# Performance work log

Measured on AMD Instinct MI355X. Metric: run time of the kernel, lower is better.

Reference implementation:

```python
import jax, jax.numpy as jnp
import numpy as np

N_HEAD = 16
SIZE_PER_HEAD = 64
NEG_BIG = 1e12


def _len_mask(lengths, T):
    # Faithful to: mask = 1 - cumsum(one_hot(len, T), 1)
    # -> 1.0 for positions < len, 0.0 for positions >= len (all ones if len == T).
    pos = jnp.arange(T)
    return (pos[None, :] < lengths[:, 0, None]).astype(jnp.float32)  # [B, T]


def setup_inputs() -> dict:
    key = jax.random.key(0)
    ks = jax.random.split(key, 8)
    B, T, D = 2, 2048, 1024
    Q_seq = jax.random.normal(ks[0], (B, T, D), dtype=jnp.float32)
    K_seq = jax.random.normal(ks[1], (B, T, D), dtype=jnp.float32)
    V_seq = jax.random.normal(ks[2], (B, T, D), dtype=jnp.float32)
    Q_len = jax.random.randint(ks[3], (B, 1), 0, T, dtype=jnp.int32)
    V_len = jax.random.randint(ks[4], (B, 1), 0, T, dtype=jnp.int32)
    s = 1.0 / np.sqrt(D)
    WQ = jax.random.normal(ks[5], (D, N_HEAD * SIZE_PER_HEAD), dtype=jnp.float32) * s
    WK = jax.random.normal(ks[6], (D, N_HEAD * SIZE_PER_HEAD), dtype=jnp.float32) * s
    WV = jax.random.normal(ks[7], (D, N_HEAD * SIZE_PER_HEAD), dtype=jnp.float32) * s
    return {"Q_seq": Q_seq, "K_seq": K_seq, "V_seq": V_seq,
            "Q_len": Q_len, "V_len": V_len, "WQ": WQ, "WK": WK, "WV": WV}


def reference(Q_seq, K_seq, V_seq, Q_len, V_len, WQ, WK, WV):
    B, Tq, _ = Q_seq.shape
    Tk = K_seq.shape[1]
    H, dh = N_HEAD, SIZE_PER_HEAD

    q = (Q_seq @ WQ).reshape(B, Tq, H, dh)  # [B,Tq,H,dh]
    k = (K_seq @ WK).reshape(B, Tk, H, dh)
    v = (V_seq @ WV).reshape(B, Tk, H, dh)

    # scaled dot-product scores [B,H,Tq,Tk]
    A = jnp.einsum('bqhd,bkhd->bhqk', q, k) / np.sqrt(dh).astype(np.float32)

    # additive key-length mask over the key axis (original: permute+mask+permute)
    kmask = _len_mask(V_len, Tk)  # [B,Tk]
    A = A - (1.0 - kmask)[:, None, None, :] * NEG_BIG
    A = jax.nn.softmax(A, axis=-1)

    O = jnp.einsum('bhqk,bkhd->bqhd', A, v).reshape(B, Tq, H * dh)

    # multiplicative query-length mask
    qmask = _len_mask(Q_len, Tq)  # [B,Tq]
    return O * qmask[:, :, None]
```

## Files before the change

### kernel.cpp

```cpp
#include <hip/hip_runtime.h>


using short8   = __attribute__((ext_vector_type(8))) short;
using floatx4  = __attribute__((ext_vector_type(4))) float;
using floatx16 = __attribute__((ext_vector_type(16))) float;
using uintx4   = __attribute__((ext_vector_type(4))) unsigned int;
using ushort4v = __attribute__((ext_vector_type(4))) unsigned short;

__device__ __forceinline__ unsigned short f2bf(float f) {
    unsigned int u = __builtin_bit_cast(unsigned int, f);
    u += 0x7fffu + ((u >> 16) & 1u);
    return (unsigned short)(u >> 16);
}

__global__ __launch_bounds__(256) void cvt_kernel(
    const float* __restrict__ Qs, const float* __restrict__ Ks,
    const float* __restrict__ Vs, const int* __restrict__ Qlen,
    const int* __restrict__ Vlen, unsigned short* __restrict__ abf)
{
    int z = blockIdx.y, row = blockIdx.x;
    int b = row >> 11, rib = row & 2047;
    int ql = Qlen[b]; int vl = Vlen[b]; int vle = vl ? vl : 2048;
    int lim = (z == 0) ? ((ql + 127) & ~127) : ((vle + 127) & ~127);
    if (rib >= lim) return;
    const float* src = (z == 0) ? Qs : ((z == 1) ? Ks : Vs);
    int t = threadIdx.x;
    float4 v = *reinterpret_cast<const float4*>(src + (size_t)row * 1024 + t * 4);
    ushort4v o;
    o[0] = f2bf(v.x); o[1] = f2bf(v.y); o[2] = f2bf(v.z); o[3] = f2bf(v.w);
    *reinterpret_cast<ushort4v*>(abf + (size_t)z * 4194304u + (size_t)row * 1024 + t * 4) = o;
}

__global__ __launch_bounds__(256) void wt_kernel(
    const float* __restrict__ W0, const float* __restrict__ W1,
    const float* __restrict__ W2, unsigned short* __restrict__ out)
{
    __shared__ float tile[64][65];
    int z = blockIdx.z;
    const float* W = (z == 0) ? W0 : ((z == 1) ? W1 : W2);
    unsigned short* O = out + (size_t)z * 1048576u;
    int r0 = blockIdx.y * 64, c0 = blockIdx.x * 64;
    int t = threadIdx.x;
#pragma unroll
    for (int i = 0; i < 16; i++) {
        int idx = t + i * 256; int r = idx >> 6, c = idx & 63;
        tile[r][c] = W[(size_t)(r0 + r) * 1024 + c0 + c];
    }
    __syncthreads();
#pragma unroll
    for (int i = 0; i < 16; i++) {
        int idx = t + i * 256; int c = idx >> 6, r = idx & 63;
        O[(size_t)(c0 + c) * 1024 + r0 + r] = f2bf(tile[r][c]);
    }
}

template <bool PRECVT>
__global__ __launch_bounds__(256) void proj_kernel(
    const float* __restrict__ Qs, const float* __restrict__ Ks,
    const float* __restrict__ Vs, const unsigned short* __restrict__ abf,
    const unsigned short* __restrict__ wt,
    const int* __restrict__ Qlen, const int* __restrict__ Vlen,
    unsigned short* __restrict__ q, unsigned short* __restrict__ k,
    unsigned short* __restrict__ vh)
{
    __shared__ alignas(16) unsigned short As[128][72];
    __shared__ alignas(16) unsigned short Bs[128][72];

    int z = blockIdx.z;
    int tid = threadIdx.x;
    int m0 = blockIdx.y * 128, n0 = blockIdx.x * 128;
    int b = m0 >> 11, rib = m0 & 2047;
    int ql = Qlen[b]; int vl = Vlen[b]; int vle = vl ? vl : 2048;
    int lim = (z == 0) ? ((ql + 127) & ~127) : ((vle + 127) & ~127);
    if (rib >= lim) return;

    const float* Af = (z == 0) ? Qs : ((z == 1) ? Ks : Vs);
    const unsigned short* Ab = abf + (size_t)z * 4194304u;
    const unsigned short* Bt = wt + (size_t)z * 1048576u;

    int w = tid >> 6, lane = tid & 63, g = lane >> 4, lr = lane & 15;
    int wr = w >> 1, wc = w & 1;

    floatx4 acc[4][4];
#pragma unroll
    for (int m = 0; m < 4; m++)
#pragma unroll
        for (int n = 0; n < 4; n++) {
#pragma unroll
            for (int r = 0; r < 4; r++) acc[m][n][r] = 0.f;
        }

    int srow = tid >> 1, scol = (tid & 1) * 32;

    short8 pa[4], pb[4];
    float4 fa[8];

    if constexpr (PRECVT) {
#pragma unroll
        for (int i = 0; i < 4; i++)
            pa[i] = *reinterpret_cast<const short8*>(Ab + (size_t)(m0 + srow) * 1024 + scol + i * 8);
    } else {
#pragma unroll
        for (int i = 0; i < 8; i++)
            fa[i] = *reinterpret_cast<const float4*>(Af + (size_t)(m0 + srow) * 1024 + scol + i * 4);
    }
#pragma unroll
    for (int i = 0; i < 4; i++)
        pb[i] = *reinterpret_cast<const short8*>(Bt + (size_t)(n0 + srow) * 1024 + scol + i * 8);

    for (int kb = 0; kb < 1024; kb += 64) {
        __syncthreads();
        if constexpr (PRECVT) {
#pragma unroll
            for (int i = 0; i < 4; i++)
                *reinterpret_cast<short8*>(&As[srow][scol + i * 8]) = pa[i];
        } else {
#pragma unroll
            for (int i = 0; i < 4; i++) {
                short8 hcv;
                hcv[0] = (short)f2bf(fa[2*i].x);   hcv[1] = (short)f2bf(fa[2*i].y);
                hcv[2] = (short)f2bf(fa[2*i].z);   hcv[3] = (short)f2bf(fa[2*i].w);
                hcv[4] = (short)f2bf(fa[2*i+1].x); hcv[5] = (short)f2bf(fa[2*i+1].y);
                hcv[6] = (short)f2bf(fa[2*i+1].z); hcv[7] = (short)f2bf(fa[2*i+1].w);
                *reinterpret_cast<short8*>(&As[srow][scol + i * 8]) = hcv;
            }
        }
#pragma unroll
        for (int i = 0; i < 4; i++)
            *reinterpret_cast<short8*>(&Bs[srow][scol + i * 8]) = pb[i];
        __syncthreads();

        if (kb + 64 < 1024) {
            if constexpr (PRECVT) {
#pragma unroll
                for (int i = 0; i < 4; i++)
                    pa[i] = *reinterpret_cast<const short8*>(Ab + (size_t)(m0 + srow) * 1024 + kb + 64 + scol + i * 8);
            } else {
#pragma unroll
                for (int i = 0; i < 8; i++)
                    fa[i] = *reinterpret_cast<const float4*>(Af + (size_t)(m0 + srow) * 1024 + kb + 64 + scol + i * 4);
            }
#pragma unroll
            for (int i = 0; i < 4; i++)
                pb[i] = *reinterpret_cast<const short8*>(Bt + (size_t)(n0 + srow) * 1024 + kb + 64 + scol + i * 8);
        }

#pragma unroll
        for (int kc = 0; kc < 2; kc++) {
            short8 af[4], bf[4];
#pragma unroll
            for (int m = 0; m < 4; m++)
                af[m] = *reinterpret_cast<const short8*>(&As[wr * 64 + m * 16 + lr][kc * 32 + g * 8]);
#pragma unroll
            for (int n = 0; n < 4; n++)
                bf[n] = *reinterpret_cast<const short8*>(&Bs[wc * 64 + n * 16 + lr][kc * 32 + g * 8]);
#pragma unroll
            for (int m = 0; m < 4; m++)
#pragma unroll
                for (int n = 0; n < 4; n++)
                    acc[m][n] = __builtin_amdgcn_mfma_f32_16x16x32_bf16(af[m], bf[n], acc[m][n], 0, 0, 0);
        }
    }

    if (z < 2) {
        unsigned short* outp = (z == 0) ? q : k;
#pragma unroll
        for (int m = 0; m < 4; m++) {
            int row0 = m0 + wr * 64 + m * 16 + g * 4;
            int tb = row0 & 2047;
            int tile = tb >> 6, rin = tb & 63;
#pragma unroll
            for (int n = 0; n < 4; n++) {
                int col = n0 + wc * 64 + n * 16 + lr;
                int hh = col >> 6, dd = col & 63;
                int cc = dd >> 4, h2 = (dd >> 3) & 1, u = dd & 7;
                size_t base = ((size_t)(b * 16 + hh) * 32 + tile) * 4096
                            + (size_t)((cc * 2 + h2) * 512) + (size_t)rin * 8 + u;
#pragma unroll
                for (int r = 0; r < 4; r++)
                    outp[base + (size_t)r * 8] = f2bf(acc[m][n][r]);
            }
        }
    } else {
#pragma unroll
        for (int m = 0; m < 4; m++) {
            int row0 = m0 + wr * 64 + m * 16 + g * 4;
            int tg = row0 & 2047;
            int tile = tg >> 6, kin = tg & 63;
            int cc = kin >> 4, h2 = (kin >> 3) & 1, u = kin & 7;
#pragma unroll
            for (int n = 0; n < 4; n++) {
                int col = n0 + wc * 64 + n * 16 + lr;
                int hh = col >> 6, dd = col & 63;
                ushort4v pk;
#pragma unroll
                for (int r = 0; r < 4; r++) pk[r] = f2bf(acc[m][n][r]);
                size_t addr = ((size_t)(b * 16 + hh) * 32 + tile) * 4096
                            + (size_t)((cc * 2 + h2) * 512) + (size_t)dd * 8 + u;
                *reinterpret_cast<ushort4v*>(vh + addr) = pk;
            }
        }
    }
}

__global__ __launch_bounds__(128) void attn_kernel(
    const unsigned short* __restrict__ q, const unsigned short* __restrict__ k,
    const unsigned short* __restrict__ vh, const int* __restrict__ Qlen,
    const int* __restrict__ Vlen, float* __restrict__ out)
{
    __shared__ float obuf[2][64][33];
    __shared__ float mlm[2][2][33];
    __shared__ float mll[2][2][33];

    int tid = threadIdx.x;
    int w = tid >> 6, lane = tid & 63;
    int j = lane & 31, hi = lane >> 5;

    int blk = blockIdx.x;
    int x = blk & 7, idx = blk >> 3;
    int bh = x + 8 * (idx >> 5), qb = idx & 31;
    int b = bh >> 4, h = bh & 15;
    int qlen = Qlen[b]; int vl = Vlen[b]; int vle = vl ? vl : 2048;

    if (qb * 64 >= qlen) {
        int zr = qb * 64 + (tid >> 1);
        float* p = out + (size_t)(b * 2048 + zr) * 1024 + h * 64 + (tid & 1) * 32;
        float4 z4; z4.x = 0.f; z4.y = 0.f; z4.z = 0.f; z4.w = 0.f;
#pragma unroll
        for (int s = 0; s < 8; s++) *reinterpret_cast<float4*>(p + 4 * s) = z4;
        return;
    }

    int nt = (vle + 63) >> 6;
    int ntw = (nt - w + 1) >> 1;

    size_t hb = (size_t)(b * 16 + h) * 131072u;
    const unsigned short* kh = k + hb;
    const unsigned short* vb = vh + hb;
    int lo = hi * 512 + j * 8;

    short8 qfA[4], qfB[4];
    {
        const unsigned short* qt = q + hb + (size_t)qb * 4096 + lo;
#pragma unroll
        for (int c = 0; c < 4; c++) {
            qfA[c] = *reinterpret_cast<const short8*>(qt + c * 1024);
            qfB[c] = *reinterpret_cast<const short8*>(qt + c * 1024 + 256);
        }
    }

    short8 kf0[4], kf1[4], vf0[4], vf1[4];
    {
        int t0 = (w < nt) ? w : (nt - 1);
        const unsigned short* kt0 = kh + (size_t)t0 * 4096 + lo;
        const unsigned short* vt0 = vb + (size_t)t0 * 4096 + lo;
#pragma unroll
        for (int c = 0; c < 4; c++) {
            kf0[c] = *reinterpret_cast<const short8*>(kt0 + c * 1024);
            kf1[c] = *reinterpret_cast<const short8*>(kt0 + c * 1024 + 256);
            vf0[c] = *reinterpret_cast<const short8*>(vt0 + c * 1024);
            vf1[c] = *reinterpret_cast<const short8*>(vt0 + c * 1024 + 256);
        }
    }
    __builtin_amdgcn_sched_barrier(0);

    floatx16 OA0, OA1, OB0, OB1;
#pragma unroll
    for (int t = 0; t < 16; t++) { OA0[t] = 0.f; OA1[t] = 0.f; OB0[t] = 0.f; OB1[t] = 0.f; }
    float mA = -3.0e38f, lA = 0.f, mB = -3.0e38f, lB = 0.f;

    const float CEXP = 0.18033688011112042f;

    for (int mi = 0; mi < ntw; ++mi) {
        int tix = w + 2 * mi;
        int kt = tix << 6;
        int tnx = tix + 2; if (tnx >= nt) tnx = nt - 1;

        floatx16 s0, s1;
#pragma unroll
        for (int t = 0; t < 16; t++) { s0[t] = 0.f; s1[t] = 0.f; }
#pragma unroll
        for (int c = 0; c < 4; c++) {
            s0 = __builtin_amdgcn_mfma_f32_32x32x16_bf16(kf0[c], qfA[c], s0, 0, 0, 0);
            s1 = __builtin_amdgcn_mfma_f32_32x32x16_bf16(kf1[c], qfA[c], s1, 0, 0, 0);
        }
        if (kt + 64 > vle) {
#pragma unroll
            for (int t = 0; t < 16; t++) {
                int kl = (t & 3) + 8 * (t >> 2) + 4 * hi;
                if (kt + kl >= vle)      s0[t] = -8.0e12f;
                if (kt + 32 + kl >= vle) s1[t] = -8.0e12f;
            }
        }
        {
            float mx = s0[0];
#pragma unroll
            for (int t = 1; t < 16; t++) mx = fmaxf(mx, s0[t]);
#pragma unroll
            for (int t = 0; t < 16; t++) mx = fmaxf(mx, s1[t]);
            float lm = fmaxf(mx, __shfl_xor(mx, 32));
            if (__any(lm > mA + 64.f)) {
                float mn = fmaxf(mA, lm);
                float al = __builtin_amdgcn_exp2f((mA - mn) * CEXP);
                mA = mn; lA *= al;
#pragma unroll
                for (int t = 0; t < 16; t++) { OA0[t] *= al; OA1[t] *= al; }
            }
            float nm = -mA * CEXP;
#pragma unroll
            for (int t = 0; t < 16; t++) {
                s0[t] = __builtin_amdgcn_exp2f(fmaf(s0[t], CEXP, nm));
                s1[t] = __builtin_amdgcn_exp2f(fmaf(s1[t], CEXP, nm));
            }
            float rs = 0.f;
#pragma unroll
            for (int t = 0; t < 16; t++) rs += s0[t] + s1[t];
            lA += rs;
        }
        {
            unsigned int pbw[4][4];
            unsigned int D[4][2];
#pragma unroll
            for (int s = 0; s < 4; s++) {
                asm("v_cvt_pk_bf16_f32 %0, %1, %2" : "=v"(D[s][0]) : "v"(s0[4*s+0]), "v"(s0[4*s+1]));
                asm("v_cvt_pk_bf16_f32 %0, %1, %2" : "=v"(D[s][1]) : "v"(s0[4*s+2]), "v"(s0[4*s+3]));
            }
#pragma unroll
            for (int u = 0; u < 2; u++) {
                asm volatile("v_permlane32_swap_b32 %0, %1" : "+v"(D[0][u]), "+v"(D[1][u]));
                asm volatile("v_permlane32_swap_b32 %0, %1" : "+v"(D[2][u]), "+v"(D[3][u]));
                pbw[0][u] = D[0][u]; pbw[0][u + 2] = D[1][u];
                pbw[1][u] = D[2][u]; pbw[1][u + 2] = D[3][u];
            }
#pragma unroll
            for (int s = 0; s < 4; s++) {
                asm("v_cvt_pk_bf16_f32 %0, %1, %2" : "=v"(D[s][0]) : "v"(s1[4*s+0]), "v"(s1[4*s+1]));
                asm("v_cvt_pk_bf16_f32 %0, %1, %2" : "=v"(D[s][1]) : "v"(s1[4*s+2]), "v"(s1[4*s+3]));
            }
#pragma unroll
            for (int u = 0; u < 2; u++) {
                asm volatile("v_permlane32_swap_b32 %0, %1" : "+v"(D[0][u]), "+v"(D[1][u]));
                asm volatile("v_permlane32_swap_b32 %0, %1" : "+v"(D[2][u]), "+v"(D[3][u]));
                pbw[2][u] = D[0][u]; pbw[2][u + 2] = D[1][u];
                pbw[3][u] = D[2][u]; pbw[3][u + 2] = D[3][u];
            }
#pragma unroll
            for (int c = 0; c < 4; c++) {
                uintx4 pw; pw[0] = pbw[c][0]; pw[1] = pbw[c][1]; pw[2] = pbw[c][2]; pw[3] = pbw[c][3];
                short8 pf = __builtin_bit_cast(short8, pw);
                OA0 = __builtin_amdgcn_mfma_f32_32x32x16_bf16(vf0[c], pf, OA0, 0, 0, 0);
                OA1 = __builtin_amdgcn_mfma_f32_32x32x16_bf16(vf1[c], pf, OA1, 0, 0, 0);
            }
        }

#pragma unroll
        for (int t = 0; t < 16; t++) { s0[t] = 0.f; s1[t] = 0.f; }
#pragma unroll
        for (int c = 0; c < 4; c++) {
            s0 = __builtin_amdgcn_mfma_f32_32x32x16_bf16(kf0[c], qfB[c], s0, 0, 0, 0);
            s1 = __builtin_amdgcn_mfma_f32_32x32x16_bf16(kf1[c], qfB[c], s1, 0, 0, 0);
        }
        {
            const unsigned short* kn = kh + (size_t)tnx * 4096 + lo;
#pragma unroll
            for (int c = 0; c < 4; c++) {
                kf0[c] = *reinterpret_cast<const short8*>(kn + c * 1024);
                kf1[c] = *reinterpret_cast<const short8*>(kn + c * 1024 + 256);
            }
        }
        __builtin_amdgcn_sched_barrier(0);

        if (kt + 64 > vle) {
#pragma unroll
            for (int t = 0; t < 16; t++) {
                int kl = (t & 3) + 8 * (t >> 2) + 4 * hi;
                if (kt + kl >= vle)      s0[t] = -8.0e12f;
                if (kt + 32 + kl >= vle) s1[t] = -8.0e12f;
            }
        }
        {
            float mx = s0[0];
#pragma unroll
            for (int t = 1; t < 16; t++) mx = fmaxf(mx, s0[t]);
#pragma unroll
            for (int t = 0; t < 16; t++) mx = fmaxf(mx, s1[t]);
            float lm = fmaxf(mx, __shfl_xor(mx, 32));
            if (__any(lm > mB + 64.f)) {
                float mn = fmaxf(mB, lm);
                float al = __builtin_amdgcn_exp2f((mB - mn) * CEXP);
                mB = mn; lB *= al;
#pragma unroll
                for (int t = 0; t < 16; t++) { OB0[t] *= al; OB1[t] *= al; }
            }
            float nm = -mB * CEXP;
#pragma unroll
            for (int t = 0; t < 16; t++) {
                s0[t] = __builtin_amdgcn_exp2f(fmaf(s0[t], CEXP, nm));
                s1[t] = __builtin_amdgcn_exp2f(fmaf(s1[t], CEXP, nm));
            }
            float rs = 0.f;
#pragma unroll
            for (int t = 0; t < 16; t++) rs += s0[t] + s1[t];
            lB += rs;
        }
        {
            unsigned int pbw[4][4];
            unsigned int D[4][2];
#pragma unroll
            for (int s = 0; s < 4; s++) {
                asm("v_cvt_pk_bf16_f32 %0, %1, %2" : "=v"(D[s][0]) : "v"(s0[4*s+0]), "v"(s0[4*s+1]));
                asm("v_cvt_pk_bf16_f32 %0, %1, %2" : "=v"(D[s][1]) : "v"(s0[4*s+2]), "v"(s0[4*s+3]));
            }
#pragma unroll
            for (int u = 0; u < 2; u++) {
                asm volatile("v_permlane32_swap_b32 %0, %1" : "+v"(D[0][u]), "+v"(D[1][u]));
                asm volatile("v_permlane32_swap_b32 %0, %1" : "+v"(D[2][u]), "+v"(D[3][u]));
                pbw[0][u] = D[0][u]; pbw[0][u + 2] = D[1][u];
                pbw[1][u] = D[2][u]; pbw[1][u + 2] = D[3][u];
            }
#pragma unroll
            for (int s = 0; s < 4; s++) {
                asm("v_cvt_pk_bf16_f32 %0, %1, %2" : "=v"(D[s][0]) : "v"(s1[4*s+0]), "v"(s1[4*s+1]));
                asm("v_cvt_pk_bf16_f32 %0, %1, %2" : "=v"(D[s][1]) : "v"(s1[4*s+2]), "v"(s1[4*s+3]));
            }
#pragma unroll
            for (int u = 0; u < 2; u++) {
                asm volatile("v_permlane32_swap_b32 %0, %1" : "+v"(D[0][u]), "+v"(D[1][u]));
                asm volatile("v_permlane32_swap_b32 %0, %1" : "+v"(D[2][u]), "+v"(D[3][u]));
                pbw[2][u] = D[0][u]; pbw[2][u + 2] = D[1][u];
                pbw[3][u] = D[2][u]; pbw[3][u + 2] = D[3][u];
            }
#pragma unroll
            for (int c = 0; c < 4; c++) {
                uintx4 pw; pw[0] = pbw[c][0]; pw[1] = pbw[c][1]; pw[2] = pbw[c][2]; pw[3] = pbw[c][3];
                short8 pf = __builtin_bit_cast(short8, pw);
                OB0 = __builtin_amdgcn_mfma_f32_32x32x16_bf16(vf0[c], pf, OB0, 0, 0, 0);
                OB1 = __builtin_amdgcn_mfma_f32_32x32x16_bf16(vf1[c], pf, OB1, 0, 0, 0);
            }
        }
        {
            const unsigned short* vn = vb + (size_t)tnx * 4096 + lo;
#pragma unroll
            for (int c = 0; c < 4; c++) {
                vf0[c] = *reinterpret_cast<const short8*>(vn + c * 1024);
                vf1[c] = *reinterpret_cast<const short8*>(vn + c * 1024 + 256);
            }
        }
        __builtin_amdgcn_sched_barrier(0);
    }

    lA = lA + __shfl_xor(lA, 32);
    lB = lB + __shfl_xor(lB, 32);
    if (hi == 0) { mlm[0][w][j] = mA; mlm[1][w][j] = mB; }
    __syncthreads();
    float MA = fmaxf(mlm[0][0][j], mlm[0][1][j]);
    float MB = fmaxf(mlm[1][0][j], mlm[1][1][j]);
    float alA = __builtin_amdgcn_exp2f((mA - MA) * CEXP);
    float alB = __builtin_amdgcn_exp2f((mB - MB) * CEXP);
#pragma unroll
    for (int t = 0; t < 16; t++) { OA0[t] *= alA; OA1[t] *= alA; OB0[t] *= alB; OB1[t] *= alB; }
    if (hi == 0) { mll[0][w][j] = lA * alA; mll[1][w][j] = lB * alB; }
    if (w == 1) {
#pragma unroll
        for (int t = 0; t < 16; t++) {
            obuf[0][lane][t]      = OA0[t];
            obuf[0][lane][t + 16] = OA1[t];
            obuf[1][lane][t]      = OB0[t];
            obuf[1][lane][t + 16] = OB1[t];
        }
    }
    __syncthreads();
    if (w == 0) {
#pragma unroll
        for (int t = 0; t < 16; t++) {
            OA0[t] += obuf[0][lane][t];
            OA1[t] += obuf[0][lane][t + 16];
            OB0[t] += obuf[1][lane][t];
            OB1[t] += obuf[1][lane][t + 16];
        }
        float ltA = mll[0][0][j] + mll[0][1][j];
        float ltB = mll[1][0][j] + mll[1][1][j];
        int qrA = qb * 64 + j, qrB = qb * 64 + 32 + j;
        float qmA = (qrA < qlen) ? (1.0f / ltA) : 0.f;
        float qmB = (qrB < qlen) ? (1.0f / ltB) : 0.f;
        float* oa = out + (size_t)(b * 2048 + qrA) * 1024 + h * 64;
        float* ob = out + (size_t)(b * 2048 + qrB) * 1024 + h * 64;
#pragma unroll
        for (int s = 0; s < 4; s++) {
            float4 v0, v1;
            v0.x = OA0[4*s+0] * qmA; v0.y = OA0[4*s+1] * qmA; v0.z = OA0[4*s+2] * qmA; v0.w = OA0[4*s+3] * qmA;
            v1.x = OA1[4*s+0] * qmA; v1.y = OA1[4*s+1] * qmA; v1.z = OA1[4*s+2] * qmA; v1.w = OA1[4*s+3] * qmA;
            *reinterpret_cast<float4*>(oa + 8 * s + 4 * hi) = v0;
            *reinterpret_cast<float4*>(oa + 32 + 8 * s + 4 * hi) = v1;
            v0.x = OB0[4*s+0] * qmB; v0.y = OB0[4*s+1] * qmB; v0.z = OB0[4*s+2] * qmB; v0.w = OB0[4*s+3] * qmB;
            v1.x = OB1[4*s+0] * qmB; v1.y = OB1[4*s+1] * qmB; v1.z = OB1[4*s+2] * qmB; v1.w = OB1[4*s+3] * qmB;
            *reinterpret_cast<float4*>(ob + 8 * s + 4 * hi) = v0;
            *reinterpret_cast<float4*>(ob + 32 + 8 * s + 4 * hi) = v1;
        }
    }
}

extern "C" void kernel_launch(void* const* d_in, const int* in_sizes, int n_in,
                              void* d_out, int out_size, void* d_ws, size_t ws_size,
                              hipStream_t stream)
{
    const float* Q_seq = (const float*)d_in[0];
    const float* K_seq = (const float*)d_in[1];
    const float* V_seq = (const float*)d_in[2];
    const int*   Q_len = (const int*)d_in[3];
    const int*   V_len = (const int*)d_in[4];
    const float* WQ    = (const float*)d_in[5];
    const float* WK    = (const float*)d_in[6];
    const float* WV    = (const float*)d_in[7];
    float* outp = (float*)d_out;

    unsigned short* wsb = (unsigned short*)d_ws;
    unsigned short* wt  = wsb;
    unsigned short* qp  = wsb + (size_t)3 * 1048576u;
    unsigned short* kp  = qp + 4194304u;
    unsigned short* vhp = kp + 4194304u;
    unsigned short* abf = vhp + 4194304u;

    size_t need = ((size_t)3 * 1048576u + 3u * 4194304u + (size_t)3 * 4194304u) * 2u;
    bool precvt = ws_size >= need;

    wt_kernel<<<dim3(16, 16, 3), 256, 0, stream>>>(WQ, WK, WV, wt);
    if (precvt) {
        cvt_kernel<<<dim3(4096, 3), 256, 0, stream>>>(Q_seq, K_seq, V_seq, Q_len, V_len, abf);
        proj_kernel<true><<<dim3(8, 32, 3), 256, 0, stream>>>(
            Q_seq, K_seq, V_seq, abf, wt, Q_len, V_len, qp, kp, vhp);
    } else {
        proj_kernel<false><<<dim3(8, 32, 3), 256, 0, stream>>>(
            Q_seq, K_seq, V_seq, nullptr, wt, Q_len, V_len, qp, kp, vhp);
    }
    attn_kernel<<<dim3(1024), 128, 0, stream>>>(qp, kp, vhp, Q_len, V_len, outp);
}
```

Baseline: 68.01 us.

## Fuse input bf16 conversion into projection GEMM and tree-reduce softmax max/sum

Removes the separate cvt_kernel pass that wrote bf16 copies of Q/K/V to workspace. The projection kernel now always loads fp32 activations and converts them inside its tile loop. This saves one launch and the extra round trip of the bf16 copy through memory, at the cost of twice the global read bytes for the A operand inside the GEMM. Separately, the attention kernel's per-row max and sum reductions are turned from serial chains into pairwise trees to shorten the dependency chains.

```diff
diff --git a/kernel.cpp b/kernel.cpp
--- a/kernel.cpp
+++ b/kernel.cpp
@@ -11,24 +11,6 @@
     unsigned int u = __builtin_bit_cast(unsigned int, f);
     u += 0x7fffu + ((u >> 16) & 1u);
     return (unsigned short)(u >> 16);
-}
-
-__global__ __launch_bounds__(256) void cvt_kernel(
-    const float* __restrict__ Qs, const float* __restrict__ Ks,
-    const float* __restrict__ Vs, const int* __restrict__ Qlen,
-    const int* __restrict__ Vlen, unsigned short* __restrict__ abf)
-{
-    int z = blockIdx.y, row = blockIdx.x;
-    int b = row >> 11, rib = row & 2047;
-    int ql = Qlen[b]; int vl = Vlen[b]; int vle = vl ? vl : 2048;
-    int lim = (z == 0) ? ((ql + 127) & ~127) : ((vle + 127) & ~127);
-    if (rib >= lim) return;
-    const float* src = (z == 0) ? Qs : ((z == 1) ? Ks : Vs);
-    int t = threadIdx.x;
-    float4 v = *reinterpret_cast<const float4*>(src + (size_t)row * 1024 + t * 4);
-    ushort4v o;
-    o[0] = f2bf(v.x); o[1] = f2bf(v.y); o[2] = f2bf(v.z); o[3] = f2bf(v.w);
-    *reinterpret_cast<ushort4v*>(abf + (size_t)z * 4194304u + (size_t)row * 1024 + t * 4) = o;
 }
 
 __global__ __launch_bounds__(256) void wt_kernel(
@@ -54,11 +36,9 @@
     }
 }
 
-template <bool PRECVT>
 __global__ __launch_bounds__(256) void proj_kernel(
     const float* __restrict__ Qs, const float* __restrict__ Ks,
-    const float* __restrict__ Vs, const unsigned short* __restrict__ abf,
-    const unsigned short* __restrict__ wt,
+    const float* __restrict__ Vs, const unsigned short* __restrict__ wt,
     const int* __restrict__ Qlen, const int* __restrict__ Vlen,
     unsigned short* __restrict__ q, unsigned short* __restrict__ k,
     unsigned short* __restrict__ vh)
@@ -75,7 +55,6 @@
     if (rib >= lim) return;
 
     const float* Af = (z == 0) ? Qs : ((z == 1) ? Ks : Vs);
-    const unsigned short* Ab = abf + (size_t)z * 4194304u;
     const unsigned short* Bt = wt + (size_t)z * 1048576u;
 
     int w = tid >> 6, lane = tid & 63, g = lane >> 4, lr = lane & 15;
@@ -92,38 +71,26 @@
 
     int srow = tid >> 1, scol = (tid & 1) * 32;
 
-    short8 pa[4], pb[4];
+    short8 pb[4];
     float4 fa[8];
 
-    if constexpr (PRECVT) {
-#pragma unroll
-        for (int i = 0; i < 4; i++)
-            pa[i] = *reinterpret_cast<const short8*>(Ab + (size_t)(m0 + srow) * 1024 + scol + i * 8);
-    } else {
-#pragma unroll
-        for (int i = 0; i < 8; i++)
-            fa[i] = *reinterpret_cast<const float4*>(Af + (size_t)(m0 + srow) * 1024 + scol + i * 4);
-    }
+#pragma unroll
+    for (int i = 0; i < 8; i++)
+        fa[i] = *reinterpret_cast<const float4*>(Af + (size_t)(m0 + srow) * 1024 + scol + i * 4);
 #pragma unroll
     for (int i = 0; i < 4; i++)
         pb[i] = *reinterpret_cast<const short8*>(Bt + (size_t)(n0 + srow) * 1024 + scol + i * 8);
 
     for (int kb = 0; kb < 1024; kb += 64) {
         __syncthreads();
-        if constexpr (PRECVT) {
-#pragma unroll
-            for (int i = 0; i < 4; i++)
-                *reinterpret_cast<short8*>(&As[srow][scol + i * 8]) = pa[i];
-        } else {
-#pragma unroll
-            for (int i = 0; i < 4; i++) {
-                short8 hcv;
-                hcv[0] = (short)f2bf(fa[2*i].x);   hcv[1] = (short)f2bf(fa[2*i].y);
-                hcv[2] = (short)f2bf(fa[2*i].z);   hcv[3] = (short)f2bf(fa[2*i].w);
-                hcv[4] = (short)f2bf(fa[2*i+1].x); hcv[5] = (short)f2bf(fa[2*i+1].y);
-                hcv[6] = (short)f2bf(fa[2*i+1].z); hcv[7] = (short)f2bf(fa[2*i+1].w);
-                *reinterpret_cast<short8*>(&As[srow][scol + i * 8]) = hcv;
-            }
+#pragma unroll
+        for (int i = 0; i < 4; i++) {
+            short8 hcv;
+            hcv[0] = (short)f2bf(fa[2*i].x);   hcv[1] = (short)f2bf(fa[2*i].y);
+            hcv[2] = (short)f2bf(fa[2*i].z);   hcv[3] = (short)f2bf(fa[2*i].w);
+            hcv[4] = (short)f2bf(fa[2*i+1].x); hcv[5] = (short)f2bf(fa[2*i+1].y);
+            hcv[6] = (short)f2bf(fa[2*i+1].z); hcv[7] = (short)f2bf(fa[2*i+1].w);
+            *reinterpret_cast<short8*>(&As[srow][scol + i * 8]) = hcv;
         }
 #pragma unroll
         for (int i = 0; i < 4; i++)
@@ -131,15 +98,9 @@
         __syncthreads();
 
         if (kb + 64 < 1024) {
-            if constexpr (PRECVT) {
-#pragma unroll
-                for (int i = 0; i < 4; i++)
-                    pa[i] = *reinterpret_cast<const short8*>(Ab + (size_t)(m0 + srow) * 1024 + kb + 64 + scol + i * 8);
-            } else {
-#pragma unroll
-                for (int i = 0; i < 8; i++)
-                    fa[i] = *reinterpret_cast<const float4*>(Af + (size_t)(m0 + srow) * 1024 + kb + 64 + scol + i * 4);
-            }
+#pragma unroll
+            for (int i = 0; i < 8; i++)
+                fa[i] = *reinterpret_cast<const float4*>(Af + (size_t)(m0 + srow) * 1024 + kb + 64 + scol + i * 4);
 #pragma unroll
             for (int i = 0; i < 4; i++)
                 pb[i] = *reinterpret_cast<const short8*>(Bt + (size_t)(n0 + srow) * 1024 + kb + 64 + scol + i * 8);
@@ -293,11 +254,14 @@
             }
         }
         {
-            float mx = s0[0];
-#pragma unroll
-            for (int t = 1; t < 16; t++) mx = fmaxf(mx, s0[t]);
-#pragma unroll
-            for (int t = 0; t < 16; t++) mx = fmaxf(mx, s1[t]);
+            float t16[16];
+#pragma unroll
+            for (int t = 0; t < 16; t++) t16[t] = fmaxf(s0[t], s1[t]);
+#pragma unroll
+            for (int t = 0; t < 8; t++) t16[t] = fmaxf(t16[t], t16[t + 8]);
+#pragma unroll
+            for (int t = 0; t < 4; t++) t16[t] = fmaxf(t16[t], t16[t + 4]);
+            float mx = fmaxf(fmaxf(t16[0], t16[1]), fmaxf(t16[2], t16[3]));
             float lm = fmaxf(mx, __shfl_xor(mx, 32));
             if (__any(lm > mA + 64.f)) {
                 float mn = fmaxf(mA, lm);
@@ -312,10 +276,14 @@
                 s0[t] = __builtin_amdgcn_exp2f(fmaf(s0[t], CEXP, nm));
                 s1[t] = __builtin_amdgcn_exp2f(fmaf(s1[t], CEXP, nm));
             }
-            float rs = 0.f;
-#pragma unroll
-            for (int t = 0; t < 16; t++) rs += s0[t] + s1[t];
-            lA += rs;
+            float a16[16];
+#pragma unroll
+            for (int t = 0; t < 16; t++) a16[t] = s0[t] + s1[t];
+#pragma unroll
+            for (int t = 0; t < 8; t++) a16[t] += a16[t + 8];
+#pragma unroll
+            for (int t = 0; t < 4; t++) a16[t] += a16[t + 4];
+            lA += (a16[0] + a16[1]) + (a16[2] + a16[3]);
         }
         {
             unsigned int pbw[4][4];
@@ -379,11 +347,14 @@
             }
         }
         {
-            float mx = s0[0];
-#pragma unroll
-            for (int t = 1; t < 16; t++) mx = fmaxf(mx, s0[t]);
-#pragma unroll
-            for (int t = 0; t < 16; t++) mx = fmaxf(mx, s1[t]);
+            float t16[16];
+#pragma unroll
+            for (int t = 0; t < 16; t++) t16[t] = fmaxf(s0[t], s1[t]);
+#pragma unroll
+            for (int t = 0; t < 8; t++) t16[t] = fmaxf(t16[t], t16[t + 8]);
+#pragma unroll
+            for (int t = 0; t < 4; t++) t16[t] = fmaxf(t16[t], t16[t + 4]);
+            float mx = fmaxf(fmaxf(t16[0], t16[1]), fmaxf(t16[2], t16[3]));
             float lm = fmaxf(mx, __shfl_xor(mx, 32));
             if (__any(lm > mB + 64.f)) {
                 float mn = fmaxf(mB, lm);
@@ -398,10 +369,14 @@
                 s0[t] = __builtin_amdgcn_exp2f(fmaf(s0[t], CEXP, nm));
                 s1[t] = __builtin_amdgcn_exp2f(fmaf(s1[t], CEXP, nm));
             }
-            float rs = 0.f;
-#pragma unroll
-            for (int t = 0; t < 16; t++) rs += s0[t] + s1[t];
-            lB += rs;
+            float a16[16];
+#pragma unroll
+            for (int t = 0; t < 16; t++) a16[t] = s0[t] + s1[t];
+#pragma unroll
+            for (int t = 0; t < 8; t++) a16[t] += a16[t + 8];
+#pragma unroll
+            for (int t = 0; t < 4; t++) a16[t] += a16[t + 4];
+            lB += (a16[0] + a16[1]) + (a16[2] + a16[3]);
         }
         {
             unsigned int pbw[4][4];
@@ -519,19 +494,9 @@
     unsigned short* qp  = wsb + (size_t)3 * 1048576u;
     unsigned short* kp  = qp + 4194304u;
     unsigned short* vhp = kp + 4194304u;
-    unsigned short* abf = vhp + 4194304u;
-
-    size_t need = ((size_t)3 * 1048576u + 3u * 4194304u + (size_t)3 * 4194304u) * 2u;
-    bool precvt = ws_size >= need;
 
     wt_kernel<<<dim3(16, 16, 3), 256, 0, stream>>>(WQ, WK, WV, wt);
-    if (precvt) {
-        cvt_kernel<<<dim3(4096, 3), 256, 0, stream>>>(Q_seq, K_seq, V_seq, Q_len, V_len, abf);
-        proj_kernel<true><<<dim3(8, 32, 3), 256, 0, stream>>>(
-            Q_seq, K_seq, V_seq, abf, wt, Q_len, V_len, qp, kp, vhp);
-    } else {
-        proj_kernel<false><<<dim3(8, 32, 3), 256, 0, stream>>>(
-            Q_seq, K_seq, V_seq, nullptr, wt, Q_len, V_len, qp, kp, vhp);
-    }
+    proj_kernel<<<dim3(8, 32, 3), 256, 0, stream>>>(
+        Q_seq, K_seq, V_seq, wt, Q_len, V_len, qp, kp, vhp);
     attn_kernel<<<dim3(1024), 128, 0, stream>>>(qp, kp, vhp, Q_len, V_len, outp);
 }
```

After: 84.47 us. 24.2% more time.
